# Kernel tuning notes

Measured on AMD Instinct MI355X. Metric: run time of the kernel, lower is better.

## Reference

```python
import jax, jax.numpy as jnp
import numpy as np

D_MODEL = 768
D_HID = 3072
D_OUT = 768
N_EXP = 8
TOP_K = 2
B, S = 2, 2048
LN_EPS = 1e-5


def setup_inputs() -> dict:
    key = jax.random.key(0)
    ks = jax.random.split(key, 10)
    sc_in = 1.0 / np.sqrt(D_MODEL)
    sc_hid = 1.0 / np.sqrt(D_HID)
    return {
        "x": jax.random.normal(ks[0], (B, S, D_MODEL), dtype=jnp.float32),
        "Wr": jax.random.normal(ks[1], (D_MODEL, N_EXP), dtype=jnp.float32) * sc_in,
        "br": jnp.zeros((N_EXP,), dtype=jnp.float32),
        "W1": jax.random.normal(ks[2], (N_EXP, D_MODEL, D_HID), dtype=jnp.float32) * sc_in,
        "b1": jnp.zeros((N_EXP, D_HID), dtype=jnp.float32),
        "W2": jax.random.normal(ks[3], (N_EXP, D_HID, D_OUT), dtype=jnp.float32) * sc_hid,
        "b2": jnp.zeros((N_EXP, D_OUT), dtype=jnp.float32),
        "ln_g": jnp.ones((D_OUT,), dtype=jnp.float32),
        "ln_b": jnp.zeros((D_OUT,), dtype=jnp.float32),
    }


def reference(x, Wr, br, W1, b1, W2, b2, ln_g, ln_b):
    # --- top-k router ---
    logits = jnp.einsum("bsd,de->bse", x, Wr) + br          # [B,S,E]
    probs = jax.nn.softmax(logits, axis=-1)
    top_vals, top_idx = jax.lax.top_k(probs, TOP_K)          # [B,S,K]
    routing_weights = top_vals / jnp.sum(top_vals, axis=-1, keepdims=True)

    # per-token weight given to each expert (0 if not selected)
    onehot = jax.nn.one_hot(top_idx, N_EXP, dtype=x.dtype)   # [B,S,K,E]
    expert_weights = jnp.einsum("bsk,bske->bse", routing_weights, onehot)

    # --- dense per-expert FFN over ALL tokens (faithful to source loop) ---
    h = jax.nn.gelu(jnp.einsum("bsd,edh->besh", x, W1) + b1[None, :, None, :])
    y = jnp.einsum("besh,eho->beso", h, W2) + b2[None, :, None, :]  # [B,E,S,O]

    # weighted combine
    out = jnp.einsum("beso,bse->bso", y, expert_weights)     # [B,S,O]

    # --- output LayerNorm ---
    mu = jnp.mean(out, axis=-1, keepdims=True)
    var = jnp.mean(jnp.square(out - mu), axis=-1, keepdims=True)
    out = (out - mu) * jax.lax.rsqrt(var + LN_EPS) * ln_g + ln_b
    return out
```

## Files before the change

kernel.cpp:

```cpp
#include <hip/hip_runtime.h>
#include <hip/hip_bf16.h>

#define TOKENS 4096
#define DMODEL 768
#define DHID   3072
#define NEXP   8
#define MAXTA  72
#define MAXTB  40

typedef __bf16 bf16x8 __attribute__((ext_vector_type(8)));
typedef float  f32x4  __attribute__((ext_vector_type(4)));
typedef unsigned short ushort_t;

#define VMCNT(n) asm volatile("s_waitcnt vmcnt(" #n ")" ::: "memory")

__device__ __forceinline__ void wg_barrier() {
    asm volatile("" ::: "memory");
    __builtin_amdgcn_s_barrier();
    asm volatile("" ::: "memory");
}

__device__ __forceinline__ float gelu_tanh(float x) {
    float z = 0.7978845608028654f * (x + 0.044715f * x * x * x);
    float t = 1.0f - 2.0f / (__expf(2.0f * z) + 1.0f);
    return 0.5f * x * (1.0f + t);
}

__device__ __forceinline__ float bf2f(ushort_t u) {
    unsigned v = ((unsigned)u) << 16;
    return __builtin_bit_cast(float, v);
}

__device__ __forceinline__ void gload16(const void* g, void* l) {
    __builtin_amdgcn_global_load_lds((const __attribute__((address_space(1))) void*)g,
                                     (__attribute__((address_space(3))) void*)l, 16, 0, 0);
}

__global__ void k_transpose_cvt(const float* __restrict__ in, ushort_t* __restrict__ out,
                                int R, int C) {
    __shared__ float tile[64 * 68];
    const int bx = blockIdx.x, by = blockIdx.y, bz = blockIdx.z;
    const float* ip = in + (size_t)bz * R * C;
    ushort_t* op = out + (size_t)bz * R * C;
    const int tid = threadIdx.x;
    {
        const int cq = tid & 15, rg = tid >> 4;
#pragma unroll
        for (int i = 0; i < 4; ++i) {
            int rl = rg + i * 16;
            float4 v = *(const float4*)(ip + (size_t)(by * 64 + rl) * C + bx * 64 + cq * 4);
            *(float4*)(&tile[rl * 68 + cq * 4]) = v;
        }
    }
    __syncthreads();
    {
        const int rq = tid & 15, cg = tid >> 4;
#pragma unroll
        for (int i = 0; i < 4; ++i) {
            int cl = cg + i * 16;
            ushort4 o;
            o.x = __builtin_bit_cast(ushort_t, (__bf16)tile[(rq * 4 + 0) * 68 + cl]);
            o.y = __builtin_bit_cast(ushort_t, (__bf16)tile[(rq * 4 + 1) * 68 + cl]);
            o.z = __builtin_bit_cast(ushort_t, (__bf16)tile[(rq * 4 + 2) * 68 + cl]);
            o.w = __builtin_bit_cast(ushort_t, (__bf16)tile[(rq * 4 + 3) * 68 + cl]);
            *(ushort4*)(op + (size_t)(bx * 64 + cl) * R + by * 64 + rq * 4) = o;
        }
    }
}

__launch_bounds__(256)
__global__ void k_router(const float* __restrict__ x, const float* __restrict__ Wr,
                         const float* __restrict__ br, int* __restrict__ cnt,
                         int* __restrict__ tok, int* __restrict__ slot,
                         float* __restrict__ wslot, ushort_t* __restrict__ xb) {
    __shared__ float WrT[NEXP * DMODEL];
    __shared__ int   te0[32], te1[32];
    __shared__ float tw0v[32], tw1v[32];
    __shared__ int   lcnt[NEXP], gbase[NEXP];

    const int tid = threadIdx.x;
    const int wv = tid >> 6, lane = tid & 63;

#pragma unroll
    for (int i = 0; i < 6; ++i) {
        int idx4 = i * 256 + tid;
        float4 v = ((const float4*)Wr)[idx4];
        int flat = idx4 * 4;
        int d = flat >> 3, e0 = flat & 7;
        WrT[(e0 + 0) * DMODEL + d] = v.x;
        WrT[(e0 + 1) * DMODEL + d] = v.y;
        WrT[(e0 + 2) * DMODEL + d] = v.z;
        WrT[(e0 + 3) * DMODEL + d] = v.w;
    }
    if (tid < NEXP) lcnt[tid] = 0;
    float brv[8];
#pragma unroll
    for (int e = 0; e < 8; ++e) brv[e] = br[e];
    __syncthreads();

#pragma unroll 1
    for (int it = 0; it < 8; ++it) {
        int t = blockIdx.x * 32 + wv * 8 + it;
        const float* xr = x + (size_t)t * DMODEL;
        float4 xv[3];
#pragma unroll
        for (int j = 0; j < 3; ++j) xv[j] = *(const float4*)(xr + (j * 64 + lane) * 4);
#pragma unroll
        for (int j = 0; j < 3; ++j) {
            int base = (j * 64 + lane) * 4;
            ushort4 o;
            o.x = __builtin_bit_cast(ushort_t, (__bf16)xv[j].x);
            o.y = __builtin_bit_cast(ushort_t, (__bf16)xv[j].y);
            o.z = __builtin_bit_cast(ushort_t, (__bf16)xv[j].z);
            o.w = __builtin_bit_cast(ushort_t, (__bf16)xv[j].w);
            *(ushort4*)(xb + (size_t)t * DMODEL + base) = o;
        }
        float lg[8];
#pragma unroll
        for (int e = 0; e < 8; ++e) {
            float s = 0.f;
#pragma unroll
            for (int j = 0; j < 3; ++j) {
                const float4 wv4 = *(const float4*)(&WrT[e * DMODEL + (j * 64 + lane) * 4]);
                s += xv[j].x * wv4.x;
                s += xv[j].y * wv4.y;
                s += xv[j].z * wv4.z;
                s += xv[j].w * wv4.w;
            }
#pragma unroll
            for (int o = 32; o > 0; o >>= 1) s += __shfl_xor(s, o);
            lg[e] = s + brv[e];
        }
        if (lane == 0) {
            int e0 = 0; float b0 = lg[0];
#pragma unroll
            for (int e = 1; e < 8; ++e) if (lg[e] > b0) { b0 = lg[e]; e0 = e; }
            int e1 = -1; float b1v = -1e30f;
#pragma unroll
            for (int e = 0; e < 8; ++e) if (e != e0 && lg[e] > b1v) { b1v = lg[e]; e1 = e; }
            float w0 = 1.f / (1.f + __expf(b1v - b0));
            float w1 = 1.f - w0;
            int lt = wv * 8 + it;
            te0[lt] = e0; te1[lt] = e1; tw0v[lt] = w0; tw1v[lt] = w1;
            wslot[2 * t] = w0; wslot[2 * t + 1] = w1;
        }
    }
    __syncthreads();

    int myE = 0, myPos = 0, myTok = 0, myK = 0;
    if (tid < 64) {
        int lt = tid >> 1; myK = tid & 1;
        myE = myK ? te1[lt] : te0[lt];
        myTok = blockIdx.x * 32 + lt;
        myPos = atomicAdd(&lcnt[myE], 1);
    }
    __syncthreads();
    if (tid < NEXP) gbase[tid] = atomicAdd(&cnt[tid], lcnt[tid]);
    __syncthreads();
    if (tid < 64) {
        int g = gbase[myE] + myPos;
        tok[myE * TOKENS + g] = myTok;
        slot[myE * TOKENS + g] = 2 * myTok + myK;
    }
}

__global__ void k_sched(const int* __restrict__ cnt, int* __restrict__ sch) {
    if (threadIdx.x == 0) {
        int base = 0, na = 0, nb = 0;
        for (int e = 0; e < NEXP; ++e) {
            sch[2 + e] = base;
            int ce = cnt[e];
            for (int m = 0; m < ce; m += 128) sch[16 + na++] = (e << 20) | m;
            for (int m = 0; m < ce; m += 256) sch[96 + nb++] = (e << 20) | m;
            base += ce;
        }
        sch[0] = na;
        sch[1] = nb;
    }
}

template<int BM, int BN, int WN, bool STAGE1>
__launch_bounds__(512)
__global__ void k_gemm8(const ushort_t* __restrict__ Abase, const int* __restrict__ tok,
                        const int* __restrict__ slot, const ushort_t* __restrict__ Wb,
                        const float* __restrict__ bias, void* __restrict__ outp,
                        const int* __restrict__ cnt, const int* __restrict__ sch) {
    constexpr int KR  = STAGE1 ? DMODEL : DHID;
    constexpr int NCn = STAGE1 ? DHID : DMODEL;
    constexpr int NT  = STAGE1 ? (DMODEL / 64) : (DHID / 2 / 64);
    constexpr int BUFB = (BM + BN) * 128;

    const int gx = gridDim.x;
    const int bx = blockIdx.x;
    const int q = gx >> 3, r = gx & 7;
    const int xcd = bx & 7;
    const int tile = (xcd < r ? xcd * (q + 1) : r * (q + 1) + (xcd - r) * q) + (bx >> 3);

    const int nT = sch[STAGE1 ? 0 : 1];
    if (tile >= nT) return;
    const int ent = sch[(STAGE1 ? 16 : 96) + tile];
    const int e = ent >> 20, m0 = ent & 0xFFFFF;
    const int ce = cnt[e];
    const int bH = sch[2 + e];
    const int n0 = blockIdx.y * BN;
    const int kbase = STAGE1 ? 0 : (int)blockIdx.z * (DHID / 2);

    __shared__ ushort_t lds[3 * (BM + BN) * 64];
    char* ldsB = (char*)lds;

    const int tid = threadIdx.x, lane = tid & 63, w = tid >> 6;
    const int wm = w / WN, wn = w % WN;
    const int wmBase = wm * 64, wnBase = wn * 64;
    const int fr = lane & 15, fg = lane >> 4;

    const ushort_t* src[6];
#pragma unroll
    for (int c = 0; c < 6; ++c) {
        int o = c * 8192 + tid * 16;
        bool isA = o < BM * 128;
        int po = isA ? o : (o - BM * 128);
        int so = po ^ (((po >> 9) & 1) << 5);
        int rrow = so >> 7, cb = so & 127;
        if (isA) {
            int gi = min(m0 + rrow, ce - 1);
            size_t arow = STAGE1 ? (size_t)tok[e * TOKENS + gi] : (size_t)(bH + gi);
            src[c] = Abase + arow * KR + kbase + (cb >> 1);
        } else {
            src[c] = Wb + ((size_t)e * NCn + n0 + rrow) * KR + kbase + (cb >> 1);
        }
    }

    auto issue3 = [&](int kt, int half) {
        char* db = ldsB + (kt % 3) * BUFB;
#pragma unroll
        for (int c = 0; c < 3; ++c) {
            int cc = half * 3 + c;
            gload16(src[cc] + kt * 64, db + cc * 8192 + w * 1024);
        }
    };
    auto loadfrag = [&](int kt, int ks, bf16x8* af, bf16x8* bf) {
        const char* ab = ldsB + (kt % 3) * BUFB;
        const char* bb = ab + BM * 128;
#pragma unroll
        for (int i = 0; i < 4; ++i) {
            int oA = (wmBase + i * 16 + fr) * 128 + ks * 64 + fg * 16;
            af[i] = *(const bf16x8*)(ab + (oA ^ (((oA >> 9) & 1) << 5)));
            int oB = (wnBase + i * 16 + fr) * 128 + ks * 64 + fg * 16;
            bf[i] = *(const bf16x8*)(bb + (oB ^ (((oB >> 9) & 1) << 5)));
        }
    };

    f32x4 acc[4][4] = {};

    issue3(0, 0); issue3(0, 1);
    issue3(1, 0); issue3(1, 1);
    VMCNT(6);
    wg_barrier();

#pragma unroll 1
    for (int kt = 0; kt < NT; ++kt) {
        {
            bf16x8 a0[4], b0[4];
            loadfrag(kt, 0, a0, b0);
            if (kt + 2 < NT) issue3(kt + 2, 0);
            wg_barrier();
            __builtin_amdgcn_s_setprio(1);
#pragma unroll
            for (int mi = 0; mi < 4; ++mi)
#pragma unroll
                for (int ni = 0; ni < 4; ++ni)
                    acc[mi][ni] = __builtin_amdgcn_mfma_f32_16x16x32_bf16(a0[mi], b0[ni], acc[mi][ni], 0, 0, 0);
            __builtin_amdgcn_s_setprio(0);
            wg_barrier();
        }
        {
            bf16x8 a1[4], b1f[4];
            loadfrag(kt, 1, a1, b1f);
            if (kt + 2 < NT) { issue3(kt + 2, 1); VMCNT(6); }
            else             { VMCNT(0); }
            wg_barrier();
            __builtin_amdgcn_s_setprio(1);
#pragma unroll
            for (int mi = 0; mi < 4; ++mi)
#pragma unroll
                for (int ni = 0; ni < 4; ++ni)
                    acc[mi][ni] = __builtin_amdgcn_mfma_f32_16x16x32_bf16(a1[mi], b1f[ni], acc[mi][ni], 0, 0, 0);
            __builtin_amdgcn_s_setprio(0);
            wg_barrier();
        }
    }

    float bv[4];
#pragma unroll
    for (int ni = 0; ni < 4; ++ni)
        bv[ni] = bias[e * NCn + n0 + wnBase + ni * 16 + fr];
#pragma unroll
    for (int mi = 0; mi < 4; ++mi) {
#pragma unroll
        for (int r4 = 0; r4 < 4; ++r4) {
            int gi = m0 + wmBase + mi * 16 + fg * 4 + r4;
            if (gi < ce) {
                if constexpr (STAGE1) {
                    size_t orow = (size_t)(bH + gi);
#pragma unroll
                    for (int ni = 0; ni < 4; ++ni) {
                        int col = n0 + wnBase + ni * 16 + fr;
                        float v = gelu_tanh(acc[mi][ni][r4] + bv[ni]);
                        ((ushort_t*)outp)[orow * DHID + col] =
                            __builtin_bit_cast(ushort_t, (__bf16)v);
                    }
                } else {
                    size_t orow = (size_t)blockIdx.z * 8192 + (size_t)slot[e * TOKENS + gi];
                    float badd = (blockIdx.z == 0) ? 1.f : 0.f;
#pragma unroll
                    for (int ni = 0; ni < 4; ++ni) {
                        int col = n0 + wnBase + ni * 16 + fr;
                        float v = acc[mi][ni][r4] + badd * bv[ni];
                        ((ushort_t*)outp)[orow * DMODEL + col] =
                            __builtin_bit_cast(ushort_t, (__bf16)v);
                    }
                }
            }
        }
    }
}

__global__ void k_ln(const ushort_t* __restrict__ Y2, const float* __restrict__ wslot,
                     const float* __restrict__ g, const float* __restrict__ b,
                     float* __restrict__ out) {
    int wv = threadIdx.x >> 6, lane = threadIdx.x & 63;
    int t = blockIdx.x * 4 + wv;
    const ushort_t* r00 = Y2 + (size_t)(2 * t) * DMODEL;
    const ushort_t* r01 = Y2 + (size_t)(8192 + 2 * t) * DMODEL;
    const ushort_t* r10 = r00 + DMODEL;
    const ushort_t* r11 = r01 + DMODEL;
    float w0 = wslot[2 * t], w1 = wslot[2 * t + 1];
    float4 v[3];
    float s = 0.f, ss = 0.f;
#pragma unroll
    for (int j = 0; j < 3; ++j) {
        int base = (j * 64 + lane) * 4;
        ushort4 a0 = *(const ushort4*)(r00 + base);
        ushort4 a1 = *(const ushort4*)(r01 + base);
        ushort4 c0 = *(const ushort4*)(r10 + base);
        ushort4 c1 = *(const ushort4*)(r11 + base);
        float4 c;
        c.x = w0 * (bf2f(a0.x) + bf2f(a1.x)) + w1 * (bf2f(c0.x) + bf2f(c1.x));
        c.y = w0 * (bf2f(a0.y) + bf2f(a1.y)) + w1 * (bf2f(c0.y) + bf2f(c1.y));
        c.z = w0 * (bf2f(a0.z) + bf2f(a1.z)) + w1 * (bf2f(c0.z) + bf2f(c1.z));
        c.w = w0 * (bf2f(a0.w) + bf2f(a1.w)) + w1 * (bf2f(c0.w) + bf2f(c1.w));
        v[j] = c;
        s  += c.x + c.y + c.z + c.w;
        ss += c.x * c.x + c.y * c.y + c.z * c.z + c.w * c.w;
    }
#pragma unroll
    for (int o = 32; o > 0; o >>= 1) { s += __shfl_xor(s, o); ss += __shfl_xor(ss, o); }
    float mu = s * (1.f / 768.f);
    float var = ss * (1.f / 768.f) - mu * mu;
    float inv = rsqrtf(var + 1e-5f);
    float* row = out + (size_t)t * DMODEL;
#pragma unroll
    for (int j = 0; j < 3; ++j) {
        int base = (j * 64 + lane) * 4;
        float4 gv = *(const float4*)(g + base);
        float4 bv = *(const float4*)(b + base);
        float4 o4;
        o4.x = (v[j].x - mu) * inv * gv.x + bv.x;
        o4.y = (v[j].y - mu) * inv * gv.y + bv.y;
        o4.z = (v[j].z - mu) * inv * gv.z + bv.z;
        o4.w = (v[j].w - mu) * inv * gv.w + bv.w;
        *(float4*)(row + base) = o4;
    }
}

extern "C" void kernel_launch(void* const* d_in, const int* in_sizes, int n_in,
                              void* d_out, int out_size, void* d_ws, size_t ws_size,
                              hipStream_t stream) {
    const float* x    = (const float*)d_in[0];
    const float* Wr   = (const float*)d_in[1];
    const float* br   = (const float*)d_in[2];
    const float* W1   = (const float*)d_in[3];
    const float* b1   = (const float*)d_in[4];
    const float* W2   = (const float*)d_in[5];
    const float* b2   = (const float*)d_in[6];
    const float* ln_g = (const float*)d_in[7];
    const float* ln_b = (const float*)d_in[8];
    float* out = (float*)d_out;

    char* ws = (char*)d_ws;
    int*      cnt   = (int*)(ws + 0);
    int*      sch   = (int*)(ws + 64);
    int*      tok   = (int*)(ws + 4096);
    int*      slot  = (int*)(ws + 135168);
    float*    wslot = (float*)(ws + 266240);
    ushort_t* xb    = (ushort_t*)(ws + 327680);
    ushort_t* W1t   = (ushort_t*)(ws + 6619136);
    ushort_t* W2t   = (ushort_t*)(ws + 44367872);
    ushort_t* H     = (ushort_t*)(ws + 82116608);
    ushort_t* Y2    = (ushort_t*)(ws + 132448256);

    hipMemsetAsync(cnt, 0, 32, stream);

    k_transpose_cvt<<<dim3(DHID / 64, DMODEL / 64, NEXP), dim3(256), 0, stream>>>(W1, W1t, DMODEL, DHID);
    k_transpose_cvt<<<dim3(DMODEL / 64, DHID / 64, NEXP), dim3(256), 0, stream>>>(W2, W2t, DHID, DMODEL);
    k_router<<<dim3(TOKENS / 32), dim3(256), 0, stream>>>(x, Wr, br, cnt, tok, slot, wslot, xb);
    k_sched<<<dim3(1), dim3(64), 0, stream>>>(cnt, sch);

    k_gemm8<128, 256, 4, true><<<dim3(MAXTA, DHID / 256, 1), dim3(512), 0, stream>>>(
        xb, tok, slot, W1t, b1, H, cnt, sch);
    k_gemm8<256, 128, 2, false><<<dim3(MAXTB, DMODEL / 128, 2), dim3(512), 0, stream>>>(
        H, tok, slot, W2t, b2, Y2, cnt, sch);

    k_ln<<<dim3(TOKENS / 4), dim3(256), 0, stream>>>(Y2, wslot, ln_g, ln_b, out);
}
```

Measured before the change: 237.5 us.

## Use 256x256 tiles with double-buffered LDS pipeline for both expert GEMMs

Both expert GEMM stages now share one 256x256 tile shape, with 8 warps each computing a 128x64 sub-tile. The LDS pipeline moves from a triple buffer to a double buffer, using a new swizzle and a loop over 64-wide k-slices that is split into four sub-steps with interleaved prefetch. Stage 1 now uses 256-row tiles, so the scheduler keeps one tile list, and the stage-2 grid shrinks in N. Larger tiles give more data reuse per block, at the cost of fewer blocks, so fewer CUs are busy, plus more accumulator registers and a hardcoded tile-to-XCD mapping.

New measurement: 201.4 us, median of 3. 1.18x faster.

```diff
diff --git a/kernel.cpp b/kernel.cpp
--- a/kernel.cpp
+++ b/kernel.cpp
@@ -5,8 +5,7 @@
 #define DMODEL 768
 #define DHID   3072
 #define NEXP   8
-#define MAXTA  72
-#define MAXTB  40
+#define MAXT   40
 
 typedef __bf16 bf16x8 __attribute__((ext_vector_type(8)));
 typedef float  f32x4  __attribute__((ext_vector_type(4)));
@@ -75,7 +74,6 @@
                          float* __restrict__ wslot, ushort_t* __restrict__ xb) {
     __shared__ float WrT[NEXP * DMODEL];
     __shared__ int   te0[32], te1[32];
-    __shared__ float tw0v[32], tw1v[32];
     __shared__ int   lcnt[NEXP], gbase[NEXP];
 
     const int tid = threadIdx.x;
@@ -141,7 +139,7 @@
             float w0 = 1.f / (1.f + __expf(b1v - b0));
             float w1 = 1.f - w0;
             int lt = wv * 8 + it;
-            te0[lt] = e0; te1[lt] = e1; tw0v[lt] = w0; tw1v[lt] = w1;
+            te0[lt] = e0; te1[lt] = e1;
             wslot[2 * t] = w0; wslot[2 * t + 1] = w1;
         }
     }
@@ -166,21 +164,79 @@
 
 __global__ void k_sched(const int* __restrict__ cnt, int* __restrict__ sch) {
     if (threadIdx.x == 0) {
-        int base = 0, na = 0, nb = 0;
+        int base = 0, n = 0;
         for (int e = 0; e < NEXP; ++e) {
             sch[2 + e] = base;
             int ce = cnt[e];
-            for (int m = 0; m < ce; m += 128) sch[16 + na++] = (e << 20) | m;
-            for (int m = 0; m < ce; m += 256) sch[96 + nb++] = (e << 20) | m;
+            for (int m = 0; m < ce; m += 256) sch[16 + n++] = (e << 20) | m;
             base += ce;
         }
-        sch[0] = na;
-        sch[1] = nb;
-    }
-}
-
-template<int BM, int BN, int WN, bool STAGE1>
-__launch_bounds__(512)
+        sch[0] = n;
+    }
+}
+
+
+#define ISSUE(c, kt1, BOFF)                                                            \
+    {                                                                                  \
+        _Pragma("unroll")                                                              \
+        for (int i_ = 0; i_ < 2; ++i_) {                                               \
+            const ushort_t* s_ = (((c) & 1) ? bPtr[i_] : aPtr[i_]) + (kt1) * 64 + (((c) >> 1) * 32); \
+            gload16(s_, ldsB + (BOFF) + (((c) & 1) ? 32768 : 0) + (((c) >> 1) * 16384) \
+                            + w * 2048 + i_ * 1024);                                   \
+        }                                                                              \
+    }
+
+#define MFMA16(NH)                                                                     \
+    __builtin_amdgcn_s_setprio(1);                                                     \
+    _Pragma("unroll")                                                                  \
+    for (int mi = 0; mi < 8; ++mi) {                                                   \
+        acc[mi][(NH)*2 + 0] = __builtin_amdgcn_mfma_f32_16x16x32_bf16(af[mi], bf[0], acc[mi][(NH)*2 + 0], 0, 0, 0); \
+        acc[mi][(NH)*2 + 1] = __builtin_amdgcn_mfma_f32_16x16x32_bf16(af[mi], bf[1], acc[mi][(NH)*2 + 1], 0, 0, 0); \
+    }                                                                                  \
+    __builtin_amdgcn_s_setprio(0);
+
+#define TILE(kt, BUFOFF, PF, LAST)                                                     \
+    {                                                                                  \
+        const char* bufL = ldsB + (BUFOFF);                                            \
+        bf16x8 af[8], bf[2];                                                           \
+                                                                 \
+        _Pragma("unroll")                                                              \
+        for (int mi = 0; mi < 8; ++mi) af[mi] = *(const bf16x8*)(bufL + abase + mi * 1024); \
+        bf[0] = *(const bf16x8*)(bufL + bbase + 0 * 1024);                             \
+        bf[1] = *(const bf16x8*)(bufL + bbase + 1 * 1024);                             \
+        if (PF) ISSUE(0, (kt) + 1, (BUFOFF) ^ 65536);                                  \
+        wg_barrier();                                                                  \
+        MFMA16(0)                                                                      \
+        wg_barrier();                                                                  \
+                                                                 \
+        bf[0] = *(const bf16x8*)(bufL + bbase + 2 * 1024);                             \
+        bf[1] = *(const bf16x8*)(bufL + bbase + 3 * 1024);                             \
+        if (PF) ISSUE(1, (kt) + 1, (BUFOFF) ^ 65536);                                  \
+        wg_barrier();                                                                  \
+        MFMA16(1)                                                                      \
+        if (LAST) { VMCNT(0); } else { VMCNT(4); }                                     \
+        wg_barrier();                                                                  \
+                                                                 \
+        _Pragma("unroll")                                                              \
+        for (int mi = 0; mi < 8; ++mi) af[mi] = *(const bf16x8*)(bufL + abase + 16384 + mi * 1024); \
+        bf[0] = *(const bf16x8*)(bufL + bbase + 16384 + 0 * 1024);                     \
+        bf[1] = *(const bf16x8*)(bufL + bbase + 16384 + 1 * 1024);                     \
+        if (PF) ISSUE(2, (kt) + 1, (BUFOFF) ^ 65536);                                  \
+        wg_barrier();                                                                  \
+        MFMA16(0)                                                                      \
+        wg_barrier();                                                                  \
+                                                                 \
+        bf[0] = *(const bf16x8*)(bufL + bbase + 16384 + 2 * 1024);                     \
+        bf[1] = *(const bf16x8*)(bufL + bbase + 16384 + 3 * 1024);                     \
+        if (PF) ISSUE(3, (kt) + 1, (BUFOFF) ^ 65536);                                  \
+        wg_barrier();                                                                  \
+        MFMA16(1)                                                                      \
+        VMCNT(4);                                                                      \
+        wg_barrier();                                                                  \
+    }
+
+template<bool STAGE1>
+__launch_bounds__(512, 1)
 __global__ void k_gemm8(const ushort_t* __restrict__ Abase, const int* __restrict__ tok,
                         const int* __restrict__ slot, const ushort_t* __restrict__ Wb,
                         const float* __restrict__ bias, void* __restrict__ outp,
@@ -188,114 +244,64 @@
     constexpr int KR  = STAGE1 ? DMODEL : DHID;
     constexpr int NCn = STAGE1 ? DHID : DMODEL;
     constexpr int NT  = STAGE1 ? (DMODEL / 64) : (DHID / 2 / 64);
-    constexpr int BUFB = (BM + BN) * 128;
-
-    const int gx = gridDim.x;
+
     const int bx = blockIdx.x;
-    const int q = gx >> 3, r = gx & 7;
-    const int xcd = bx & 7;
-    const int tile = (xcd < r ? xcd * (q + 1) : r * (q + 1) + (xcd - r) * q) + (bx >> 3);
-
-    const int nT = sch[STAGE1 ? 0 : 1];
+    const int tile = (bx & 7) * 5 + (bx >> 3);
+    const int nT = sch[0];
     if (tile >= nT) return;
-    const int ent = sch[(STAGE1 ? 16 : 96) + tile];
+    const int ent = sch[16 + tile];
     const int e = ent >> 20, m0 = ent & 0xFFFFF;
     const int ce = cnt[e];
     const int bH = sch[2 + e];
-    const int n0 = blockIdx.y * BN;
+    const int n0 = blockIdx.y * 256;
     const int kbase = STAGE1 ? 0 : (int)blockIdx.z * (DHID / 2);
 
-    __shared__ ushort_t lds[3 * (BM + BN) * 64];
+    __shared__ ushort_t lds[65536];
     char* ldsB = (char*)lds;
 
     const int tid = threadIdx.x, lane = tid & 63, w = tid >> 6;
-    const int wm = w / WN, wn = w % WN;
-    const int wmBase = wm * 64, wnBase = wn * 64;
+    const int wm = w >> 2, wn = w & 3;
+    const int wmBase = wm * 128, wnBase = wn * 64;
     const int fr = lane & 15, fg = lane >> 4;
 
-    const ushort_t* src[6];
-#pragma unroll
-    for (int c = 0; c < 6; ++c) {
-        int o = c * 8192 + tid * 16;
-        bool isA = o < BM * 128;
-        int po = isA ? o : (o - BM * 128);
-        int so = po ^ (((po >> 9) & 1) << 5);
-        int rrow = so >> 7, cb = so & 127;
-        if (isA) {
-            int gi = min(m0 + rrow, ce - 1);
-            size_t arow = STAGE1 ? (size_t)tok[e * TOKENS + gi] : (size_t)(bH + gi);
-            src[c] = Abase + arow * KR + kbase + (cb >> 1);
-        } else {
-            src[c] = Wb + ((size_t)e * NCn + n0 + rrow) * KR + kbase + (cb >> 1);
-        }
-    }
-
-    auto issue3 = [&](int kt, int half) {
-        char* db = ldsB + (kt % 3) * BUFB;
-#pragma unroll
-        for (int c = 0; c < 3; ++c) {
-            int cc = half * 3 + c;
-            gload16(src[cc] + kt * 64, db + cc * 8192 + w * 1024);
-        }
-    };
-    auto loadfrag = [&](int kt, int ks, bf16x8* af, bf16x8* bf) {
-        const char* ab = ldsB + (kt % 3) * BUFB;
-        const char* bb = ab + BM * 128;
-#pragma unroll
-        for (int i = 0; i < 4; ++i) {
-            int oA = (wmBase + i * 16 + fr) * 128 + ks * 64 + fg * 16;
-            af[i] = *(const bf16x8*)(ab + (oA ^ (((oA >> 9) & 1) << 5)));
-            int oB = (wnBase + i * 16 + fr) * 128 + ks * 64 + fg * 16;
-            bf[i] = *(const bf16x8*)(bb + (oB ^ (((oB >> 9) & 1) << 5)));
-        }
-    };
-
-    f32x4 acc[4][4] = {};
-
-    issue3(0, 0); issue3(0, 1);
-    issue3(1, 0); issue3(1, 1);
-    VMCNT(6);
+    const ushort_t* aPtr[2];
+    const ushort_t* bPtr[2];
+#pragma unroll
+    for (int i = 0; i < 2; ++i) {
+        int j = w * 2 + i;
+        int row = j * 16 + (lane >> 2);
+        int gblk = (lane & 3) ^ ((row >> 1) & 3);
+        int gi = min(m0 + row, ce - 1);
+        size_t ar = STAGE1 ? (size_t)tok[e * TOKENS + gi] : (size_t)(bH + gi);
+        aPtr[i] = Abase + ar * KR + kbase + gblk * 8;
+        bPtr[i] = Wb + ((size_t)e * NCn + n0 + row) * KR + kbase + gblk * 8;
+    }
+
+    const int arow0 = wmBase + fr;
+    const int abase = arow0 * 64 + ((fg ^ ((arow0 >> 1) & 3)) << 4);
+    const int brow0 = wnBase + fr;
+    const int bbase = 32768 + brow0 * 64 + ((fg ^ ((brow0 >> 1) & 3)) << 4);
+
+    f32x4 acc[8][4] = {};
+
+    ISSUE(0, 0, 0); ISSUE(1, 0, 0); ISSUE(2, 0, 0); ISSUE(3, 0, 0);
+    VMCNT(4);
     wg_barrier();
 
 #pragma unroll 1
-    for (int kt = 0; kt < NT; ++kt) {
-        {
-            bf16x8 a0[4], b0[4];
-            loadfrag(kt, 0, a0, b0);
-            if (kt + 2 < NT) issue3(kt + 2, 0);
-            wg_barrier();
-            __builtin_amdgcn_s_setprio(1);
-#pragma unroll
-            for (int mi = 0; mi < 4; ++mi)
-#pragma unroll
-                for (int ni = 0; ni < 4; ++ni)
-                    acc[mi][ni] = __builtin_amdgcn_mfma_f32_16x16x32_bf16(a0[mi], b0[ni], acc[mi][ni], 0, 0, 0);
-            __builtin_amdgcn_s_setprio(0);
-            wg_barrier();
-        }
-        {
-            bf16x8 a1[4], b1f[4];
-            loadfrag(kt, 1, a1, b1f);
-            if (kt + 2 < NT) { issue3(kt + 2, 1); VMCNT(6); }
-            else             { VMCNT(0); }
-            wg_barrier();
-            __builtin_amdgcn_s_setprio(1);
-#pragma unroll
-            for (int mi = 0; mi < 4; ++mi)
-#pragma unroll
-                for (int ni = 0; ni < 4; ++ni)
-                    acc[mi][ni] = __builtin_amdgcn_mfma_f32_16x16x32_bf16(a1[mi], b1f[ni], acc[mi][ni], 0, 0, 0);
-            __builtin_amdgcn_s_setprio(0);
-            wg_barrier();
-        }
-    }
+    for (int kt = 0; kt < NT - 2; kt += 2) {
+        TILE(kt, 0, 1, 0)
+        TILE(kt + 1, 65536, 1, 0)
+    }
+    TILE(NT - 2, 0, 1, 0)
+    TILE(NT - 1, 65536, 0, 1)
 
     float bv[4];
 #pragma unroll
     for (int ni = 0; ni < 4; ++ni)
         bv[ni] = bias[e * NCn + n0 + wnBase + ni * 16 + fr];
 #pragma unroll
-    for (int mi = 0; mi < 4; ++mi) {
+    for (int mi = 0; mi < 8; ++mi) {
 #pragma unroll
         for (int r4 = 0; r4 < 4; ++r4) {
             int gi = m0 + wmBase + mi * 16 + fg * 4 + r4;
@@ -406,9 +412,9 @@
     k_router<<<dim3(TOKENS / 32), dim3(256), 0, stream>>>(x, Wr, br, cnt, tok, slot, wslot, xb);
     k_sched<<<dim3(1), dim3(64), 0, stream>>>(cnt, sch);
 
-    k_gemm8<128, 256, 4, true><<<dim3(MAXTA, DHID / 256, 1), dim3(512), 0, stream>>>(
+    k_gemm8<true><<<dim3(MAXT, DHID / 256, 1), dim3(512), 0, stream>>>(
         xb, tok, slot, W1t, b1, H, cnt, sch);
-    k_gemm8<256, 128, 2, false><<<dim3(MAXTB, DMODEL / 128, 2), dim3(512), 0, stream>>>(
+    k_gemm8<false><<<dim3(MAXT, DMODEL / 256, 2), dim3(512), 0, stream>>>(
         H, tok, slot, W2t, b2, Y2, cnt, sch);
 
     k_ln<<<dim3(TOKENS / 4), dim3(256), 0, stream>>>(Y2, wslot, ln_g, ln_b, out);
```
